# Performance work log

Measured on AMD Instinct MI355X. Metric: run time of the kernel, lower is better.

Reference implementation:

```python
import jax, jax.numpy as jnp
import numpy as np

N = 100_000      # nodes
E = 1_600_000    # edges (avg degree 16)
D_IN, D_HID, D_OUT = 128, 64, 64
NEG_SLOPE = 0.2  # PyG GATConv default


def setup_inputs() -> dict:
    key = jax.random.key(0)
    ks = jax.random.split(key, 10)
    s = lambda k, shape: jax.random.normal(k, shape, jnp.float32) * 0.1
    return {
        "x": jax.random.normal(ks[0], (N, D_IN), jnp.float32),
        "edge_index": jax.random.randint(ks[1], (2, E), 0, N, dtype=jnp.int32),
        "W1": s(ks[2], (D_IN, D_HID)),
        "a_src1": s(ks[3], (D_HID,)),
        "a_dst1": s(ks[4], (D_HID,)),
        "b1": jnp.zeros((D_HID,), jnp.float32),
        "W2": s(ks[5], (D_HID, D_OUT)),
        "a_src2": s(ks[6], (D_OUT,)),
        "a_dst2": s(ks[7], (D_OUT,)),
        "b2": jnp.zeros((D_OUT,), jnp.float32),
    }


def gat_conv(x, src, dst, W, a_src, a_dst, b):
    """Single-head PyG-style GATConv (self-loops already appended to src/dst)."""
    n = x.shape[0]
    h = x @ W                                   # [N, D]
    # per-edge attention logits: leaky_relu(a_src . h_j + a_dst . h_i)
    logit = jax.nn.leaky_relu((h @ a_src)[src] + (h @ a_dst)[dst], NEG_SLOPE)
    # segment softmax over incoming edges of each dst node
    m = jax.ops.segment_max(logit, dst, num_segments=n)
    e = jnp.exp(logit - m[dst])
    denom = jax.ops.segment_sum(e, dst, num_segments=n)
    alpha = e / (denom[dst] + 1e-16)            # [E]
    out = jax.ops.segment_sum(alpha[:, None] * h[src], dst, num_segments=n)
    return out + b


def reference(x, edge_index, W1, a_src1, a_dst1, b1, W2, a_src2, a_dst2, b2):
    n = x.shape[0]
    loops = jnp.arange(n, dtype=edge_index.dtype)  # add_self_loops=True default
    src = jnp.concatenate([edge_index[0], loops])
    dst = jnp.concatenate([edge_index[1], loops])
    h = gat_conv(x, src, dst, W1, a_src1, a_dst1, b1)
    embedding = jax.nn.relu(h)   # dropout = identity (inference semantics)
    out = gat_conv(embedding, src, dst, W2, a_src2, a_dst2, b2)
    return (embedding, out)
```

## Files before the change

kernel.cpp:

```cpp
#include <hip/hip_runtime.h>
#include <hip/hip_bf16.h>

#define DHID 64
#define SUBSH 9
#define SUBSZ (1 << SUBSH)
#define PCAP 16384
#define EB 2048
typedef __attribute__((ext_vector_type(8))) short short8;
typedef __attribute__((ext_vector_type(4))) float f32x4;

static __device__ __forceinline__ short tobf(float f) {
  __hip_bfloat16 h = __float2bfloat16(f);
  return *reinterpret_cast<short*>(&h);
}

__global__ __launch_bounds__(256)
void k_fusedA(const int* __restrict__ src, const int* __restrict__ dst,
              int* __restrict__ bkt, int* __restrict__ bcnt,
              int E, int nsb, int cap, int nbkt,
              const float* __restrict__ xf, const float* __restrict__ W1,
              const float* __restrict__ a_s, const float* __restrict__ a_d,
              short* __restrict__ hb, float* __restrict__ asb,
              float* __restrict__ adb, int N) {
  __shared__ int lcnt[256];
  __shared__ int lbase[256];
  __shared__ __align__(16) short ldsB[64 * 128];
  int tid = threadIdx.x;
  if (blockIdx.x < nbkt) {
    int c0 = blockIdx.x * EB;
    for (int i = tid; i < nsb; i += 256) lcnt[i] = 0;
    __syncthreads();
    int wloc[8], uloc[8], rloc[8];
    #pragma unroll
    for (int k = 0; k < 8; k++) {
      int i = c0 + tid + k * 256;
      if (i < E) {
        int d = dst[i];
        int w = d >> SUBSH;
        wloc[k] = w;
        uloc[k] = (src[i] << SUBSH) | (d & (SUBSZ - 1));
        rloc[k] = atomicAdd(&lcnt[w], 1);
      } else wloc[k] = -1;
    }
    __syncthreads();
    for (int i = tid; i < nsb; i += 256) lbase[i] = atomicAdd(&bcnt[i], lcnt[i]);
    __syncthreads();
    #pragma unroll
    for (int k = 0; k < 8; k++) {
      int w = wloc[k];
      if (w >= 0) bkt[(size_t)w * cap + lbase[w] + rloc[k]] = uloc[k];
    }
    return;
  }
  int n0 = (blockIdx.x - nbkt) * 64;
  for (int e = tid; e < 128 * 64; e += 256) {
    int k = e >> 6, c = e & 63;
    ldsB[c * 128 + (k ^ ((c & 7) << 3))] = tobf(W1[e]);
  }
  __syncthreads();

  int l = tid & 63, w = tid >> 6;
  int c = l & 15, g = l >> 4;
  f32x4 acc[4];
  #pragma unroll
  for (int t = 0; t < 4; t++) acc[t] = (f32x4){0.f, 0.f, 0.f, 0.f};

  int arow = 16 * w + c;
  int row0 = n0 + arow;
  const float* xr = xf + (size_t)row0 * 128;
  bool okr = row0 < N;
  short8 afr[4];
  #pragma unroll
  for (int s = 0; s < 4; s++) {
    int ke = s * 32 + g * 8;
    float4 u0 = make_float4(0.f, 0.f, 0.f, 0.f), u1 = u0;
    if (okr) { u0 = *(const float4*)(xr + ke); u1 = *(const float4*)(xr + ke + 4); }
    short8 af;
    af[0] = tobf(u0.x); af[1] = tobf(u0.y); af[2] = tobf(u0.z); af[3] = tobf(u0.w);
    af[4] = tobf(u1.x); af[5] = tobf(u1.y); af[6] = tobf(u1.z); af[7] = tobf(u1.w);
    afr[s] = af;
  }
  #pragma unroll
  for (int s = 0; s < 4; s++) {
    int ke = s * 32 + g * 8;
    #pragma unroll
    for (int t = 0; t < 4; t++) {
      int bcol = 16 * t + c;
      short8 bf = *(const short8*)(ldsB + bcol * 128 + (ke ^ ((bcol & 7) << 3)));
      acc[t] = __builtin_amdgcn_mfma_f32_16x16x32_bf16(afr[s], bf, acc[t], 0, 0, 0);
    }
  }
  float av_s[4], av_d[4];
  #pragma unroll
  for (int t = 0; t < 4; t++) { av_s[t] = a_s[16 * t + c]; av_d[t] = a_d[16 * t + c]; }
  #pragma unroll
  for (int q = 0; q < 4; q++) {
    int row = n0 + 16 * w + g * 4 + q;
    bool ok = row < N;
    float rs = 0.f, rd = 0.f;
    #pragma unroll
    for (int t = 0; t < 4; t++) {
      float v = acc[t][q];
      if (ok) hb[(size_t)row * 64 + 16 * t + c] = tobf(v);
      rs += v * av_s[t]; rd += v * av_d[t];
    }
    #pragma unroll
    for (int off = 1; off < 16; off <<= 1) {
      rs += __shfl_xor(rs, off, 64);
      rd += __shfl_xor(rd, off, 64);
    }
    if (ok && c == 0) { asb[row] = rs; adb[row] = rd; }
  }
}

__global__ __launch_bounds__(256)
void k_place2(const int* __restrict__ bkt, const int* __restrict__ bcnt,
              int* __restrict__ roff, int* __restrict__ csr,
              int N, int nsb, int cap) {
  __shared__ int scanbuf[256];
  __shared__ int h[SUBSZ];
  __shared__ int roff_l[SUBSZ + 1];
  __shared__ int lcnt[SUBSZ];
  __shared__ int stage[PCAP];
  __shared__ int sbase;
  int sb = blockIdx.x, tid = threadIdx.x;
  int d0 = sb << SUBSH;
  int nn = min(N - d0, SUBSZ);

  int tot = 0;
  if (tid < nsb) tot = bcnt[tid] + min(N - (tid << SUBSH), SUBSZ);
  scanbuf[tid] = tot; __syncthreads();
  for (int off = 1; off < 256; off <<= 1) {
    int t = (tid >= off) ? scanbuf[tid - off] : 0;
    __syncthreads(); scanbuf[tid] += t; __syncthreads();
  }
  if (tid == sb) sbase = scanbuf[tid] - tot;
  __syncthreads();

  for (int j = tid; j < SUBSZ; j += 256) { h[j] = 1; lcnt[j] = 0; }
  __syncthreads();
  int nE = bcnt[sb];
  const int* b = bkt + (size_t)sb * cap;
  for (int i = tid; i < nE; i += 256) atomicAdd(&h[b[i] & (SUBSZ - 1)], 1);
  __syncthreads();

  int a0 = h[2 * tid], a1 = h[2 * tid + 1];
  int s = a0 + a1;
  scanbuf[tid] = s; __syncthreads();
  for (int off = 1; off < 256; off <<= 1) {
    int t = (tid >= off) ? scanbuf[tid - off] : 0;
    __syncthreads(); scanbuf[tid] += t; __syncthreads();
  }
  int excl = sbase + scanbuf[tid] - s;
  roff_l[2 * tid] = excl;
  roff_l[2 * tid + 1] = excl + a0;
  if (tid == 255) roff_l[SUBSZ] = sbase + scanbuf[255];
  __syncthreads();

  for (int j = tid; j < nn; j += 256) roff[d0 + j] = roff_l[j];
  if (d0 + nn == N && tid == 0) roff[N] = roff_l[nn];

  int base0 = roff_l[0];
  int span = roff_l[nn] - base0;
  if (span <= PCAP) {
    for (int d = tid; d < nn; d += 256) stage[roff_l[d] - base0] = (d0 + d) << 7;
    for (int i = tid; i < nE; i += 256) {
      int u = b[i];
      int dl = u & (SUBSZ - 1);
      int rk = 1 + atomicAdd(&lcnt[dl], 1);
      stage[roff_l[dl] - base0 + rk] = (u >> SUBSH) << 7;
    }
    __syncthreads();
    for (int j = tid; j < span; j += 256) csr[base0 + j] = stage[j];
  } else {
    for (int d = tid; d < nn; d += 256) csr[roff_l[d]] = (d0 + d) << 7;
    for (int i = tid; i < nE; i += 256) {
      int u = b[i];
      int dl = u & (SUBSZ - 1);
      int rk = 1 + atomicAdd(&lcnt[dl], 1);
      csr[roff_l[dl] + rk] = (u >> SUBSH) << 7;
    }
  }
}

__global__ __launch_bounds__(256)
void k_mgemm2(const short* __restrict__ eb, const float* __restrict__ W2,
              const float* __restrict__ a_s, const float* __restrict__ a_d,
              short* __restrict__ hb, float* __restrict__ asb,
              float* __restrict__ adb, int N) {
  __shared__ __align__(16) short lds[64 * 64 * 2];
  int tid = threadIdx.x;
  int n0 = blockIdx.x * 64;
  const char* ga = (const char*)eb + (size_t)n0 * 128;
  #pragma unroll
  for (int j = 0; j < 2; j++) {
    int d = j * 4096 + tid * 16;
    __builtin_amdgcn_global_load_lds(
        (__attribute__((address_space(1))) const void*)(ga + d),
        (__attribute__((address_space(3))) void*)((char*)lds + d), 16, 0, 0);
  }
  short* B = lds + 64 * 64;
  for (int e = tid; e < 64 * 64; e += 256) {
    int k = e >> 6, c = e & 63;
    B[c * 64 + (k ^ ((c & 7) << 3))] = tobf(W2[e]);
  }
  __syncthreads();

  int l = tid & 63, w = tid >> 6;
  int c = l & 15, g = l >> 4;
  const short* A = lds;
  f32x4 acc[4];
  #pragma unroll
  for (int t = 0; t < 4; t++) acc[t] = (f32x4){0.f, 0.f, 0.f, 0.f};
  int arow = 16 * w + c;
  #pragma unroll
  for (int s = 0; s < 2; s++) {
    int ke = s * 32 + g * 8;
    short8 af = *(const short8*)(A + arow * 64 + (ke ^ ((arow & 7) << 3)));
    #pragma unroll
    for (int t = 0; t < 4; t++) {
      int bcol = 16 * t + c;
      short8 bf = *(const short8*)(B + bcol * 64 + (ke ^ ((bcol & 7) << 3)));
      acc[t] = __builtin_amdgcn_mfma_f32_16x16x32_bf16(af, bf, acc[t], 0, 0, 0);
    }
  }
  float av_s[4], av_d[4];
  #pragma unroll
  for (int t = 0; t < 4; t++) { av_s[t] = a_s[16 * t + c]; av_d[t] = a_d[16 * t + c]; }
  #pragma unroll
  for (int q = 0; q < 4; q++) {
    int row = n0 + 16 * w + g * 4 + q;
    bool ok = row < N;
    float rs = 0.f, rd = 0.f;
    #pragma unroll
    for (int t = 0; t < 4; t++) {
      float v = acc[t][q];
      if (ok) hb[(size_t)row * 64 + 16 * t + c] = tobf(v);
      rs += v * av_s[t]; rd += v * av_d[t];
    }
    #pragma unroll
    for (int off = 1; off < 16; off <<= 1) {
      rs += __shfl_xor(rs, off, 64);
      rd += __shfl_xor(rd, off, 64);
    }
    if (ok && c == 0) { asb[row] = rs; adb[row] = rd; }
  }
}

__global__ void k_agg(const int* __restrict__ roff, const int* __restrict__ csr,
                      const float* __restrict__ asb, const float* __restrict__ adb,
                      const short* __restrict__ hb, const float* __restrict__ b,
                      float* __restrict__ out, short* __restrict__ outb,
                      int N, int relu) {
  const char* hbase = (const char*)hb;
  int lane = threadIdx.x & 63;
  int colb = (lane & 15) * 8;
  int L = lane & 15;
  int wid = blockIdx.x * (blockDim.x >> 6) + (threadIdx.x >> 6);
  int nw = gridDim.x * (blockDim.x >> 6);
  float4 bv4 = ((const float4*)b)[L];

  int r0c = 0, r1c = 0, sc = 0, r0n = 0, r1n = 0, sn = 0;
  float adc = 0.f, avc = 0.f, adn = 0.f;
  if (wid < N) {
    r0c = roff[wid]; r1c = roff[wid + 1]; adc = adb[wid];
    if (lane < min(64, r1c - r0c)) sc = csr[r0c + lane];
    avc = asb[sc >> 7];
  }
  if (wid + nw < N) {
    r0n = roff[wid + nw]; r1n = roff[wid + nw + 1]; adn = adb[wid + nw];
    if (lane < min(64, r1n - r0n)) sn = csr[r0n + lane];
  }

  for (int n = wid; n < N; n += nw) {
    int cnt0 = min(64, r1c - r0c);
    float e = 0.f;
    if (lane < cnt0) {
      float l = avc + adc;
      l = fmaxf(l, 0.2f * l);
      e = __expf(l);
    }
    int n2 = n + 2 * nw;
    int r02 = 0, r12 = 0; float ad2 = 0.f;
    if (n2 < N) { r02 = roff[n2]; r12 = roff[n2 + 1]; ad2 = adb[n2]; }
    float avn = asb[sn >> 7];

    float a0 = 0.f, a1 = 0.f, a2 = 0.f, a3 = 0.f, denl = e;
    {
      int cntUp = (cnt0 + 3) & ~3;
      int addrv = (lane >> 4) << 2;
      #pragma unroll 4
      for (int j = 0; j < cntUp; j += 4) {
        int sofs = __builtin_amdgcn_ds_bpermute(addrv, sc);
        int ewi  = __builtin_amdgcn_ds_bpermute(addrv, (int)__float_as_uint(e));
        addrv += 16;
        float ew = __uint_as_float((unsigned)ewi);
        uint2 u = *(const uint2*)(hbase + (unsigned)(sofs + colb));
        a0 = fmaf(__uint_as_float(u.x << 16), ew, a0);
        a1 = fmaf(__uint_as_float(u.x & 0xFFFF0000u), ew, a1);
        a2 = fmaf(__uint_as_float(u.y << 16), ew, a2);
        a3 = fmaf(__uint_as_float(u.y & 0xFFFF0000u), ew, a3);
      }
    }
    for (int base = r0c + 64; base < r1c; base += 64) {
      int cnt = min(64, r1c - base);
      int s128 = 0; float e2 = 0.f;
      if (lane < cnt) {
        s128 = csr[base + lane];
        float l = asb[s128 >> 7] + adc;
        l = fmaxf(l, 0.2f * l);
        e2 = __expf(l);
      }
      denl += e2;
      int cntUp = (cnt + 3) & ~3;
      int addrv = (lane >> 4) << 2;
      for (int j = 0; j < cntUp; j += 4) {
        int sofs = __builtin_amdgcn_ds_bpermute(addrv, s128);
        int ewi  = __builtin_amdgcn_ds_bpermute(addrv, (int)__float_as_uint(e2));
        addrv += 16;
        float ew = __uint_as_float((unsigned)ewi);
        uint2 u = *(const uint2*)(hbase + (unsigned)(sofs + colb));
        a0 = fmaf(__uint_as_float(u.x << 16), ew, a0);
        a1 = fmaf(__uint_as_float(u.x & 0xFFFF0000u), ew, a1);
        a2 = fmaf(__uint_as_float(u.y << 16), ew, a2);
        a3 = fmaf(__uint_as_float(u.y & 0xFFFF0000u), ew, a3);
      }
    }
    #pragma unroll
    for (int off = 16; off <= 32; off <<= 1) {
      a0 += __shfl_xor(a0, off, 64); a1 += __shfl_xor(a1, off, 64);
      a2 += __shfl_xor(a2, off, 64); a3 += __shfl_xor(a3, off, 64);
    }
    float den = denl;
    #pragma unroll
    for (int off = 32; off; off >>= 1) den += __shfl_xor(den, off, 64);
    float inv = 1.f / (den + 1e-16f);
    if (lane < 16) {
      float4 o;
      o.x = fmaf(a0, inv, bv4.x); o.y = fmaf(a1, inv, bv4.y);
      o.z = fmaf(a2, inv, bv4.z); o.w = fmaf(a3, inv, bv4.w);
      if (relu) {
        o.x = fmaxf(o.x, 0.f); o.y = fmaxf(o.y, 0.f);
        o.z = fmaxf(o.z, 0.f); o.w = fmaxf(o.w, 0.f);
      }
      ((float4*)(out + (size_t)n * DHID))[L] = o;
      if (outb) {
        short4 ob = make_short4(tobf(o.x), tobf(o.y), tobf(o.z), tobf(o.w));
        ((short4*)(outb + (size_t)n * DHID))[L ^ ((n & 7) << 1)] = ob;
      }
    }
    r0c = r0n; r1c = r1n; adc = adn; sc = sn; avc = avn;
    r0n = r02; r1n = r12; adn = ad2;
    sn = 0;
    if (n2 < N && lane < min(64, r1n - r0n)) sn = csr[r0n + lane];
  }
}

extern "C" void kernel_launch(void* const* d_in, const int* in_sizes, int n_in,
                              void* d_out, int out_size, void* d_ws, size_t ws_size,
                              hipStream_t stream) {
  const float* x   = (const float*)d_in[0];
  const int*   ei  = (const int*)d_in[1];
  const float* W1  = (const float*)d_in[2];
  const float* as1 = (const float*)d_in[3];
  const float* ad1 = (const float*)d_in[4];
  const float* b1  = (const float*)d_in[5];
  const float* W2  = (const float*)d_in[6];
  const float* as2 = (const float*)d_in[7];
  const float* ad2 = (const float*)d_in[8];
  const float* b2  = (const float*)d_in[9];

  int N = in_sizes[0] / 128;
  int E = in_sizes[1] / 2;
  const int* srcp = ei;
  const int* dstp = ei + E;

  float* emb  = (float*)d_out;
  float* out2 = emb + (size_t)N * DHID;

  char* w = (char*)d_ws;
  auto alloc = [&](size_t bytes) { char* p = w; w += (bytes + 255) & ~(size_t)255; return p; };
  int NR = ((N + 63) / 64) * 64;
  int* roff = (int*)alloc((size_t)(N + 1) * 4);
  int* csr  = (int*)alloc((size_t)(E + N) * 4);
  int* bcnt = (int*)alloc(1024);
  char* scr0 = alloc((size_t)NR * 128 * 2);
  short* hb = (short*)alloc((size_t)NR * 64 * 2);
  float* asb = (float*)alloc((size_t)N * 4);
  float* adb = (float*)alloc((size_t)N * 4);
  short* eb = (short*)scr0;
  int* bkt  = (int*)scr0;

  int nsb = (N + SUBSZ - 1) >> SUBSH;
  int cap = E / nsb + 4096;

  int NBLK = (N + 63) / 64;
  int nbkt = (E + EB - 1) / EB;

  hipMemsetAsync(bcnt, 0, (size_t)nsb * 4, stream);
  k_fusedA<<<nbkt + NBLK, 256, 0, stream>>>(srcp, dstp, bkt, bcnt, E, nsb, cap, nbkt,
                                            x, W1, as1, ad1, hb, asb, adb, N);
  k_place2<<<nsb, 256, 0, stream>>>(bkt, bcnt, roff, csr, N, nsb, cap);

  k_agg<<<2048, 256, 0, stream>>>(roff, csr, asb, adb, hb, b1, emb, eb, N, 1);
  k_mgemm2<<<NBLK, 256, 0, stream>>>(eb, W2, as2, ad2, hb, asb, adb, N);
  k_agg<<<2048, 256, 0, stream>>>(roff, csr, asb, adb, hb, b2, out2, (short*)nullptr, N, 0);
}
```

Baseline: 164.0 us.

## Fuse layer-1 attention aggregation with layer-2 GEMM through shared memory

Replaces the separate layer-1 aggregation and layer-2 MFMA GEMM kernels with one kernel. Each block aggregates 64 destination nodes, one wave per 16 nodes, and writes the ReLU'd bf16 embedding rows straight into LDS, then runs the W2 MFMA and attention-projection epilogue from there. This removes the global round trip of the bf16 embedding and one kernel launch. Because the layer-1 feature buffer is still being read, the layer-2 features and logit vectors go to separate buffers. The cost is a fixed per-wave node assignment in place of the grid-stride schedule, which can add degree-driven load imbalance within a block.

```diff
diff --git a/kernel.cpp b/kernel.cpp
--- a/kernel.cpp
+++ b/kernel.cpp
@@ -184,31 +184,130 @@
 }
 
 __global__ __launch_bounds__(256)
-void k_mgemm2(const short* __restrict__ eb, const float* __restrict__ W2,
-              const float* __restrict__ a_s, const float* __restrict__ a_d,
-              short* __restrict__ hb, float* __restrict__ asb,
-              float* __restrict__ adb, int N) {
-  __shared__ __align__(16) short lds[64 * 64 * 2];
+void k_aggGemm(const int* __restrict__ roff, const int* __restrict__ csr,
+               const float* __restrict__ asb, const float* __restrict__ adb,
+               const short* __restrict__ hb, const float* __restrict__ b1v,
+               float* __restrict__ emb,
+               const float* __restrict__ W2,
+               const float* __restrict__ a_s2, const float* __restrict__ a_d2,
+               short* __restrict__ hb2, float* __restrict__ asb2,
+               float* __restrict__ adb2, int N) {
+  __shared__ __align__(16) short ldsA[64 * 64];
+  __shared__ __align__(16) short ldsB[64 * 64];
+  const char* hbase = (const char*)hb;
   int tid = threadIdx.x;
   int n0 = blockIdx.x * 64;
-  const char* ga = (const char*)eb + (size_t)n0 * 128;
-  #pragma unroll
-  for (int j = 0; j < 2; j++) {
-    int d = j * 4096 + tid * 16;
-    __builtin_amdgcn_global_load_lds(
-        (__attribute__((address_space(1))) const void*)(ga + d),
-        (__attribute__((address_space(3))) void*)((char*)lds + d), 16, 0, 0);
-  }
-  short* B = lds + 64 * 64;
+  int lane = tid & 63, w = tid >> 6;
+
   for (int e = tid; e < 64 * 64; e += 256) {
     int k = e >> 6, c = e & 63;
-    B[c * 64 + (k ^ ((c & 7) << 3))] = tobf(W2[e]);
+    ldsB[c * 64 + (k ^ ((c & 7) << 3))] = tobf(W2[e]);
+  }
+
+  {
+    int colb = (lane & 15) * 8;
+    int L = lane & 15;
+    float4 bv4 = ((const float4*)b1v)[L];
+    int nbase = n0 + w * 16;
+
+    int r0c = 0, r1c = 0, sc = 0, r0n = 0, r1n = 0, sn = 0;
+    float adc = 0.f, avc = 0.f, adn = 0.f;
+    if (nbase < N) {
+      r0c = roff[nbase]; r1c = roff[nbase + 1]; adc = adb[nbase];
+      if (lane < min(64, r1c - r0c)) sc = csr[r0c + lane];
+      avc = asb[sc >> 7];
+    }
+    if (nbase + 1 < N) {
+      r0n = roff[nbase + 1]; r1n = roff[nbase + 2]; adn = adb[nbase + 1];
+      if (lane < min(64, r1n - r0n)) sn = csr[r0n + lane];
+    }
+
+    for (int i = 0; i < 16; i++) {
+      int n = nbase + i;
+      if (n >= N) break;
+      int cnt0 = min(64, r1c - r0c);
+      float e = 0.f;
+      if (lane < cnt0) {
+        float l = avc + adc;
+        l = fmaxf(l, 0.2f * l);
+        e = __expf(l);
+      }
+      int n2 = n + 2;
+      int r02 = 0, r12 = 0; float ad2v = 0.f;
+      bool p2 = (i + 2 < 16) && (n2 < N);
+      if (p2) { r02 = roff[n2]; r12 = roff[n2 + 1]; ad2v = adb[n2]; }
+      float avn = asb[sn >> 7];
+
+      float a0 = 0.f, a1 = 0.f, a2 = 0.f, a3 = 0.f, denl = e;
+      {
+        int cntUp = (cnt0 + 3) & ~3;
+        int addrv = (lane >> 4) << 2;
+        #pragma unroll 4
+        for (int j = 0; j < cntUp; j += 4) {
+          int sofs = __builtin_amdgcn_ds_bpermute(addrv, sc);
+          int ewi  = __builtin_amdgcn_ds_bpermute(addrv, (int)__float_as_uint(e));
+          addrv += 16;
+          float ew = __uint_as_float((unsigned)ewi);
+          uint2 u = *(const uint2*)(hbase + (unsigned)(sofs + colb));
+          a0 = fmaf(__uint_as_float(u.x << 16), ew, a0);
+          a1 = fmaf(__uint_as_float(u.x & 0xFFFF0000u), ew, a1);
+          a2 = fmaf(__uint_as_float(u.y << 16), ew, a2);
+          a3 = fmaf(__uint_as_float(u.y & 0xFFFF0000u), ew, a3);
+        }
+      }
+      for (int base = r0c + 64; base < r1c; base += 64) {
+        int cnt = min(64, r1c - base);
+        int s128 = 0; float e2 = 0.f;
+        if (lane < cnt) {
+          s128 = csr[base + lane];
+          float l = asb[s128 >> 7] + adc;
+          l = fmaxf(l, 0.2f * l);
+          e2 = __expf(l);
+        }
+        denl += e2;
+        int cntUp = (cnt + 3) & ~3;
+        int addrv = (lane >> 4) << 2;
+        for (int j = 0; j < cntUp; j += 4) {
+          int sofs = __builtin_amdgcn_ds_bpermute(addrv, s128);
+          int ewi  = __builtin_amdgcn_ds_bpermute(addrv, (int)__float_as_uint(e2));
+          addrv += 16;
+          float ew = __uint_as_float((unsigned)ewi);
+          uint2 u = *(const uint2*)(hbase + (unsigned)(sofs + colb));
+          a0 = fmaf(__uint_as_float(u.x << 16), ew, a0);
+          a1 = fmaf(__uint_as_float(u.x & 0xFFFF0000u), ew, a1);
+          a2 = fmaf(__uint_as_float(u.y << 16), ew, a2);
+          a3 = fmaf(__uint_as_float(u.y & 0xFFFF0000u), ew, a3);
+        }
+      }
+      #pragma unroll
+      for (int off = 16; off <= 32; off <<= 1) {
+        a0 += __shfl_xor(a0, off, 64); a1 += __shfl_xor(a1, off, 64);
+        a2 += __shfl_xor(a2, off, 64); a3 += __shfl_xor(a3, off, 64);
+      }
+      float den = denl;
+      #pragma unroll
+      for (int off = 32; off; off >>= 1) den += __shfl_xor(den, off, 64);
+      float inv = 1.f / (den + 1e-16f);
+      if (lane < 16) {
+        float4 o;
+        o.x = fmaxf(fmaf(a0, inv, bv4.x), 0.f);
+        o.y = fmaxf(fmaf(a1, inv, bv4.y), 0.f);
+        o.z = fmaxf(fmaf(a2, inv, bv4.z), 0.f);
+        o.w = fmaxf(fmaf(a3, inv, bv4.w), 0.f);
+        ((float4*)(emb + (size_t)n * DHID))[L] = o;
+        int lrow = n - n0;
+        short4 ob = make_short4(tobf(o.x), tobf(o.y), tobf(o.z), tobf(o.w));
+        ((short4*)(ldsA + lrow * 64))[L ^ ((lrow & 7) << 1)] = ob;
+      }
+      r0c = r0n; r1c = r1n; adc = adn; sc = sn; avc = avn;
+      r0n = r02; r1n = r12; adn = ad2v;
+      sn = 0;
+      if (p2 && lane < min(64, r1n - r0n)) sn = csr[r0n + lane];
+    }
   }
   __syncthreads();
 
-  int l = tid & 63, w = tid >> 6;
-  int c = l & 15, g = l >> 4;
-  const short* A = lds;
+  int c = lane & 15, g = lane >> 4;
   f32x4 acc[4];
   #pragma unroll
   for (int t = 0; t < 4; t++) acc[t] = (f32x4){0.f, 0.f, 0.f, 0.f};
@@ -216,17 +315,17 @@
   #pragma unroll
   for (int s = 0; s < 2; s++) {
     int ke = s * 32 + g * 8;
-    short8 af = *(const short8*)(A + arow * 64 + (ke ^ ((arow & 7) << 3)));
+    short8 af = *(const short8*)(ldsA + arow * 64 + (ke ^ ((arow & 7) << 3)));
     #pragma unroll
     for (int t = 0; t < 4; t++) {
       int bcol = 16 * t + c;
-      short8 bf = *(const short8*)(B + bcol * 64 + (ke ^ ((bcol & 7) << 3)));
+      short8 bf = *(const short8*)(ldsB + bcol * 64 + (ke ^ ((bcol & 7) << 3)));
       acc[t] = __builtin_amdgcn_mfma_f32_16x16x32_bf16(af, bf, acc[t], 0, 0, 0);
     }
   }
   float av_s[4], av_d[4];
   #pragma unroll
-  for (int t = 0; t < 4; t++) { av_s[t] = a_s[16 * t + c]; av_d[t] = a_d[16 * t + c]; }
+  for (int t = 0; t < 4; t++) { av_s[t] = a_s2[16 * t + c]; av_d[t] = a_d2[16 * t + c]; }
   #pragma unroll
   for (int q = 0; q < 4; q++) {
     int row = n0 + 16 * w + g * 4 + q;
@@ -235,7 +334,7 @@
     #pragma unroll
     for (int t = 0; t < 4; t++) {
       float v = acc[t][q];
-      if (ok) hb[(size_t)row * 64 + 16 * t + c] = tobf(v);
+      if (ok) hb2[(size_t)row * 64 + 16 * t + c] = tobf(v);
       rs += v * av_s[t]; rd += v * av_d[t];
     }
     #pragma unroll
@@ -243,15 +342,14 @@
       rs += __shfl_xor(rs, off, 64);
       rd += __shfl_xor(rd, off, 64);
     }
-    if (ok && c == 0) { asb[row] = rs; adb[row] = rd; }
+    if (ok && c == 0) { asb2[row] = rs; adb2[row] = rd; }
   }
 }
 
 __global__ void k_agg(const int* __restrict__ roff, const int* __restrict__ csr,
                       const float* __restrict__ asb, const float* __restrict__ adb,
                       const short* __restrict__ hb, const float* __restrict__ b,
-                      float* __restrict__ out, short* __restrict__ outb,
-                      int N, int relu) {
+                      float* __restrict__ out, int N) {
   const char* hbase = (const char*)hb;
   int lane = threadIdx.x & 63;
   int colb = (lane & 15) * 8;
@@ -339,15 +437,7 @@
       float4 o;
       o.x = fmaf(a0, inv, bv4.x); o.y = fmaf(a1, inv, bv4.y);
       o.z = fmaf(a2, inv, bv4.z); o.w = fmaf(a3, inv, bv4.w);
-      if (relu) {
-        o.x = fmaxf(o.x, 0.f); o.y = fmaxf(o.y, 0.f);
-        o.z = fmaxf(o.z, 0.f); o.w = fmaxf(o.w, 0.f);
-      }
       ((float4*)(out + (size_t)n * DHID))[L] = o;
-      if (outb) {
-        short4 ob = make_short4(tobf(o.x), tobf(o.y), tobf(o.z), tobf(o.w));
-        ((short4*)(outb + (size_t)n * DHID))[L ^ ((n & 7) << 1)] = ob;
-      }
     }
     r0c = r0n; r1c = r1n; adc = adn; sc = sn; avc = avn;
     r0n = r02; r1n = r12; adn = ad2;
@@ -388,7 +478,9 @@
   short* hb = (short*)alloc((size_t)NR * 64 * 2);
   float* asb = (float*)alloc((size_t)N * 4);
   float* adb = (float*)alloc((size_t)N * 4);
-  short* eb = (short*)scr0;
+  float* asb2 = (float*)alloc((size_t)N * 4);
+  float* adb2 = (float*)alloc((size_t)N * 4);
+  short* hb2 = (short*)scr0;
   int* bkt  = (int*)scr0;
 
   int nsb = (N + SUBSZ - 1) >> SUBSH;
@@ -402,7 +494,7 @@
                                             x, W1, as1, ad1, hb, asb, adb, N);
   k_place2<<<nsb, 256, 0, stream>>>(bkt, bcnt, roff, csr, N, nsb, cap);
 
-  k_agg<<<2048, 256, 0, stream>>>(roff, csr, asb, adb, hb, b1, emb, eb, N, 1);
-  k_mgemm2<<<NBLK, 256, 0, stream>>>(eb, W2, as2, ad2, hb, asb, adb, N);
-  k_agg<<<2048, 256, 0, stream>>>(roff, csr, asb, adb, hb, b2, out2, (short*)nullptr, N, 0);
+  k_aggGemm<<<NBLK, 256, 0, stream>>>(roff, csr, asb, adb, hb, b1, emb,
+                                      W2, as2, ad2, hb2, asb2, adb2, N);
+  k_agg<<<2048, 256, 0, stream>>>(roff, csr, asb2, adb2, hb2, b2, out2, N);
 }
```

Measured after the change: 202.1 us. 1.23x slower.

## Feed layer-2 GEMM from fp32 embedding and double bucket chunk size

Applied to the files above, without the earlier changes.

The first aggregation no longer writes a swizzled bf16 copy of the embedding. The layer-2 GEMM now reads the fp32 embedding directly from global memory and converts it to bf16 in registers. Layer-2 features and attention scalars go to separate buffers (hb2 reuses the scratch space), removing the in-place overwrite of layer-1 buffers. The edge-bucketing chunk per block is doubled to 4096, halving the bucket block count while raising register use. The change trades an extra bf16 write pass for a wider fp32 read in the GEMM.

```diff
diff --git a/kernel.cpp b/kernel.cpp
--- a/kernel.cpp
+++ b/kernel.cpp
@@ -5,7 +5,7 @@
 #define SUBSH 9
 #define SUBSZ (1 << SUBSH)
 #define PCAP 16384
-#define EB 2048
+#define EB 4096
 typedef __attribute__((ext_vector_type(8))) short short8;
 typedef __attribute__((ext_vector_type(4))) float f32x4;
 
@@ -30,9 +30,9 @@
     int c0 = blockIdx.x * EB;
     for (int i = tid; i < nsb; i += 256) lcnt[i] = 0;
     __syncthreads();
-    int wloc[8], uloc[8], rloc[8];
-    #pragma unroll
-    for (int k = 0; k < 8; k++) {
+    int wloc[16], uloc[16], rloc[16];
+    #pragma unroll
+    for (int k = 0; k < 16; k++) {
       int i = c0 + tid + k * 256;
       if (i < E) {
         int d = dst[i];
@@ -46,7 +46,7 @@
     for (int i = tid; i < nsb; i += 256) lbase[i] = atomicAdd(&bcnt[i], lcnt[i]);
     __syncthreads();
     #pragma unroll
-    for (int k = 0; k < 8; k++) {
+    for (int k = 0; k < 16; k++) {
       int w = wloc[k];
       if (w >= 0) bkt[(size_t)w * cap + lbase[w] + rloc[k]] = uloc[k];
     }
@@ -184,44 +184,47 @@
 }
 
 __global__ __launch_bounds__(256)
-void k_mgemm2(const short* __restrict__ eb, const float* __restrict__ W2,
+void k_mgemm2(const float* __restrict__ emb, const float* __restrict__ W2,
               const float* __restrict__ a_s, const float* __restrict__ a_d,
               short* __restrict__ hb, float* __restrict__ asb,
               float* __restrict__ adb, int N) {
-  __shared__ __align__(16) short lds[64 * 64 * 2];
+  __shared__ __align__(16) short ldsB[64 * 64];
   int tid = threadIdx.x;
   int n0 = blockIdx.x * 64;
-  const char* ga = (const char*)eb + (size_t)n0 * 128;
-  #pragma unroll
-  for (int j = 0; j < 2; j++) {
-    int d = j * 4096 + tid * 16;
-    __builtin_amdgcn_global_load_lds(
-        (__attribute__((address_space(1))) const void*)(ga + d),
-        (__attribute__((address_space(3))) void*)((char*)lds + d), 16, 0, 0);
-  }
-  short* B = lds + 64 * 64;
   for (int e = tid; e < 64 * 64; e += 256) {
     int k = e >> 6, c = e & 63;
-    B[c * 64 + (k ^ ((c & 7) << 3))] = tobf(W2[e]);
+    ldsB[c * 64 + (k ^ ((c & 7) << 3))] = tobf(W2[e]);
   }
   __syncthreads();
 
   int l = tid & 63, w = tid >> 6;
   int c = l & 15, g = l >> 4;
-  const short* A = lds;
   f32x4 acc[4];
   #pragma unroll
   for (int t = 0; t < 4; t++) acc[t] = (f32x4){0.f, 0.f, 0.f, 0.f};
   int arow = 16 * w + c;
+  int row0 = n0 + arow;
+  const float* xr = emb + (size_t)row0 * 64;
+  bool okr = row0 < N;
+  short8 afr[2];
   #pragma unroll
   for (int s = 0; s < 2; s++) {
     int ke = s * 32 + g * 8;
-    short8 af = *(const short8*)(A + arow * 64 + (ke ^ ((arow & 7) << 3)));
+    float4 u0 = make_float4(0.f, 0.f, 0.f, 0.f), u1 = u0;
+    if (okr) { u0 = *(const float4*)(xr + ke); u1 = *(const float4*)(xr + ke + 4); }
+    short8 af;
+    af[0] = tobf(u0.x); af[1] = tobf(u0.y); af[2] = tobf(u0.z); af[3] = tobf(u0.w);
+    af[4] = tobf(u1.x); af[5] = tobf(u1.y); af[6] = tobf(u1.z); af[7] = tobf(u1.w);
+    afr[s] = af;
+  }
+  #pragma unroll
+  for (int s = 0; s < 2; s++) {
+    int ke = s * 32 + g * 8;
     #pragma unroll
     for (int t = 0; t < 4; t++) {
       int bcol = 16 * t + c;
-      short8 bf = *(const short8*)(B + bcol * 64 + (ke ^ ((bcol & 7) << 3)));
-      acc[t] = __builtin_amdgcn_mfma_f32_16x16x32_bf16(af, bf, acc[t], 0, 0, 0);
+      short8 bf = *(const short8*)(ldsB + bcol * 64 + (ke ^ ((bcol & 7) << 3)));
+      acc[t] = __builtin_amdgcn_mfma_f32_16x16x32_bf16(afr[s], bf, acc[t], 0, 0, 0);
     }
   }
   float av_s[4], av_d[4];
@@ -250,8 +253,7 @@
 __global__ void k_agg(const int* __restrict__ roff, const int* __restrict__ csr,
                       const float* __restrict__ asb, const float* __restrict__ adb,
                       const short* __restrict__ hb, const float* __restrict__ b,
-                      float* __restrict__ out, short* __restrict__ outb,
-                      int N, int relu) {
+                      float* __restrict__ out, int N, int relu) {
   const char* hbase = (const char*)hb;
   int lane = threadIdx.x & 63;
   int colb = (lane & 15) * 8;
@@ -344,10 +346,6 @@
         o.z = fmaxf(o.z, 0.f); o.w = fmaxf(o.w, 0.f);
       }
       ((float4*)(out + (size_t)n * DHID))[L] = o;
-      if (outb) {
-        short4 ob = make_short4(tobf(o.x), tobf(o.y), tobf(o.z), tobf(o.w));
-        ((short4*)(outb + (size_t)n * DHID))[L ^ ((n & 7) << 1)] = ob;
-      }
     }
     r0c = r0n; r1c = r1n; adc = adn; sc = sn; avc = avn;
     r0n = r02; r1n = r12; adn = ad2;
@@ -388,7 +386,9 @@
   short* hb = (short*)alloc((size_t)NR * 64 * 2);
   float* asb = (float*)alloc((size_t)N * 4);
   float* adb = (float*)alloc((size_t)N * 4);
-  short* eb = (short*)scr0;
+  float* asb2 = (float*)alloc((size_t)N * 4);
+  float* adb2 = (float*)alloc((size_t)N * 4);
+  short* hb2 = (short*)scr0;
   int* bkt  = (int*)scr0;
 
   int nsb = (N + SUBSZ - 1) >> SUBSH;
@@ -402,7 +402,7 @@
                                             x, W1, as1, ad1, hb, asb, adb, N);
   k_place2<<<nsb, 256, 0, stream>>>(bkt, bcnt, roff, csr, N, nsb, cap);
 
-  k_agg<<<2048, 256, 0, stream>>>(roff, csr, asb, adb, hb, b1, emb, eb, N, 1);
-  k_mgemm2<<<NBLK, 256, 0, stream>>>(eb, W2, as2, ad2, hb, asb, adb, N);
-  k_agg<<<2048, 256, 0, stream>>>(roff, csr, asb, adb, hb, b2, out2, (short*)nullptr, N, 0);
-}
+  k_agg<<<2048, 256, 0, stream>>>(roff, csr, asb, adb, hb, b1, emb, N, 1);
+  k_mgemm2<<<NBLK, 256, 0, stream>>>(emb, W2, as2, ad2, hb2, asb2, adb2, N);
+  k_agg<<<2048, 256, 0, stream>>>(roff, csr, asb2, adb2, hb2, b2, out2, N, 0);
+}
```

New measurement: 156.0 us. -4.9%, faster.
